# Kernel optimization log

Measured on AMD Instinct MI355X. Metric: run time of the kernel, lower is better.

## Reference

```python
import math
import jax, jax.numpy as jnp
import numpy as np

B = 65536
EMBED = 256
COND = 256
TIME = 128
HID = 256
E = 8
RHID = 128
IN_DIM = EMBED + TIME + COND  # 640


def setup_inputs() -> dict:
    key = jax.random.key(0)
    ks = jax.random.split(key, 20)
    s = 0.02
    inp = {
        "z_t": jax.random.normal(ks[0], (B, EMBED), jnp.float32),
        "t": jax.random.uniform(ks[1], (B, 1), jnp.float32),
        "cond": jax.random.normal(ks[2], (B, COND), jnp.float32),
        # time embedding proj (Linear(time,time) -> SiLU -> Linear(time,time))
        "tW1": jax.random.normal(ks[3], (TIME, TIME), jnp.float32) * s,
        "tb1": jnp.zeros((TIME,), jnp.float32),
        "tW2": jax.random.normal(ks[4], (TIME, TIME), jnp.float32) * s,
        "tb2": jnp.zeros((TIME,), jnp.float32),
        # stacked expert weights [E, in, out]
        "eW1": jax.random.normal(ks[5], (E, IN_DIM, HID), jnp.float32) * s,
        "eb1": jnp.zeros((E, HID), jnp.float32),
        "eW2": jax.random.normal(ks[6], (E, HID, HID), jnp.float32) * s,
        "eb2": jnp.zeros((E, HID), jnp.float32),
        "eW3": jax.random.normal(ks[7], (E, HID, EMBED), jnp.float32) * s,
        "eb3": jnp.zeros((E, EMBED), jnp.float32),
        # router
        "rW1": jax.random.normal(ks[8], (IN_DIM, RHID), jnp.float32) * s,
        "rb1": jnp.zeros((RHID,), jnp.float32),
        "rW2": jax.random.normal(ks[9], (RHID, E), jnp.float32) * s,
        "rb2": jnp.zeros((E,), jnp.float32),
    }
    return inp


def _time_embedding(t, tW1, tb1, tW2, tb2):
    half = TIME // 2  # 64
    scale = -math.log(10000.0) / (half - 1)
    freqs = jnp.exp(jnp.arange(half, dtype=t.dtype) * scale)[None, :]  # [1, half]
    angles = t * freqs  # [B, half]
    emb = jnp.concatenate([jnp.sin(angles), jnp.cos(angles)], axis=-1)  # [B, TIME]
    h = jax.nn.silu(emb @ tW1 + tb1)
    return h @ tW2 + tb2


def reference(z_t, t, cond, tW1, tb1, tW2, tb2, eW1, eb1, eW2, eb2, eW3, eb3, rW1, rb1, rW2, rb2):
    time_emb = _time_embedding(t, tW1, tb1, tW2, tb2)
    x = jnp.concatenate([z_t, time_emb, cond], axis=-1)  # [B, IN_DIM]
    # dense MoE: all experts via batched GEMMs (dropout=0 -> identity)
    h1 = jax.nn.silu(jnp.einsum('bi,eih->beh', x, eW1) + eb1)      # [B,E,HID]
    h2 = jax.nn.silu(jnp.einsum('beh,ehk->bek', h1, eW2) + eb2)    # [B,E,HID]
    expert_out = jnp.einsum('beh,ehd->bed', h2, eW3) + eb3         # [B,E,EMBED]
    # router softmax gate
    rh = jax.nn.silu(x @ rW1 + rb1)
    gate = jax.nn.softmax(rh @ rW2 + rb2, axis=-1)                 # [B,E]
    velocity = jnp.einsum('be,bed->bd', gate, expert_out)          # [B,EMBED]
    return velocity, gate
```

## Files before the change

kernel.cpp:

```cpp
#include <hip/hip_runtime.h>

typedef __attribute__((ext_vector_type(8))) short bf16x8;
typedef __attribute__((ext_vector_type(4))) float f32x4;

#define NB_ROWS 65536
#define D_EMBED 256
#define D_HID   256
#define N_EXP   8
#define D_RHID  128
#define D_IN    640
#define D_H1    2048

#define HSTR 264

static __device__ __forceinline__ ushort f2bf(float f) {
  union { float f; unsigned u; } v; v.f = f;
  unsigned r = v.u + 0x7fffu + ((v.u >> 16) & 1u);
  return (ushort)(r >> 16);
}
static __device__ __forceinline__ float bf2f(ushort h) {
  union { unsigned u; float f; } v; v.u = ((unsigned)h) << 16;
  return v.f;
}
static __device__ __forceinline__ float silu_f(float x) {
  return x / (1.0f + __expf(-x));
}

static __device__ __forceinline__ int kswz(int r, int c) {
  return r * 64 + ((((c) >> 3) ^ (r & 7)) << 3) + ((c) & 7);
}
static __device__ __forceinline__ int gswz(int r, int c) {
  return ((c) & ~63) | (((((c) >> 3) & 7) ^ ((r) & 7)) << 3) | ((c) & 7);
}

static __device__ __forceinline__ void gl16(const ushort* src, ushort* dst) {
  __builtin_amdgcn_global_load_lds(
      (const __attribute__((address_space(1))) void*)src,
      (__attribute__((address_space(3))) void*)dst, 16, 0, 0);
}

__global__ void prep_all(const float* __restrict__ tW1, const float* __restrict__ tW2,
                         const float* __restrict__ rW1, const float* __restrict__ eW1,
                         const float* __restrict__ eW2, const float* __restrict__ eW3,
                         ushort* __restrict__ tw1t, ushort* __restrict__ tw2t,
                         ushort* __restrict__ rw1t, ushort* __restrict__ w1t,
                         ushort* __restrict__ w2t, ushort* __restrict__ w3t) {
  int gidx = blockIdx.x * 256 + threadIdx.x;
  if (gidx >= 2473984) return;
  const float* src; ushort* dst; int R, C; int swz; int idx;
  if (gidx < 16384)        { src = tW1; dst = tw1t; R = 128; C = 128; swz = 0; idx = gidx; }
  else if (gidx < 32768)   { src = tW2; dst = tw2t; R = 128; C = 128; swz = 0; idx = gidx - 16384; }
  else if (gidx < 114688)  { src = rW1; dst = rw1t; R = 640; C = 128; swz = 1; idx = gidx - 32768; }
  else if (gidx < 1425408) { src = eW1; dst = w1t;  R = 640; C = 256; swz = 1; idx = gidx - 114688; }
  else if (gidx < 1949696) { src = eW2; dst = w2t;  R = 256; C = 256; swz = 1; idx = gidx - 1425408; }
  else                     { src = eW3; dst = w3t;  R = 256; C = 256; swz = 1; idx = gidx - 1949696; }
  int rc = R * C;
  int m = idx / rc;
  int rem = idx - m * rc;
  int r = rem / C;
  int c = rem - r * C;
  int p = swz ? ((r & ~63) + (((((r >> 3) & 7) ^ (c & 7)) << 3) | (r & 7))) : r;
  dst[m * rc + c * R + p] = f2bf(src[idx]);
}

static __device__ __forceinline__ void glB128_256(const ushort* __restrict__ src, int ld,
                                                  int kt, ushort* dst, int tid, int w) {
  #pragma unroll
  for (int c = 0; c < 4; ++c) {
    int f = c * 4096 + tid * 16;
    int r = f >> 7, ce = (f & 127) >> 1;
    gl16(src + (size_t)r * ld + kt + ce, dst + ((c * 4096 + w * 1024) >> 1));
  }
}

__global__ __launch_bounds__(512) void time_x_kernel(
    const float* __restrict__ zt, const float* __restrict__ tin,
    const float* __restrict__ cond,
    const ushort* __restrict__ tw1t, const ushort* __restrict__ tw2t,
    const float* __restrict__ tb1, const float* __restrict__ tb2,
    ushort* __restrict__ x) {
  __shared__ __align__(16) ushort sE[128 * 136];
  __shared__ float sFreq[64];
  __shared__ float sB1[128];
  __shared__ float sB2[128];

  const int tid = threadIdx.x;
  const int row0 = blockIdx.x * 128;

  for (int ch = tid; ch < 128 * 64; ch += 512) {
    int r = ch >> 6;
    int c4 = (ch & 63) << 2;
    size_t grow = (size_t)(row0 + r);
    float4 zv = *(const float4*)&zt[grow * 256 + c4];
    ushort4 o; o.x = f2bf(zv.x); o.y = f2bf(zv.y); o.z = f2bf(zv.z); o.w = f2bf(zv.w);
    *(ushort4*)&x[grow * 640 + gswz(r, c4)] = o;
    float4 cv = *(const float4*)&cond[grow * 256 + c4];
    ushort4 o2; o2.x = f2bf(cv.x); o2.y = f2bf(cv.y); o2.z = f2bf(cv.z); o2.w = f2bf(cv.w);
    *(ushort4*)&x[grow * 640 + gswz(r, 384 + c4)] = o2;
  }

  if (tid < 64) sFreq[tid] = __expf((float)tid * (-9.210340371976184f / 63.0f));
  if (tid < 128) { sB1[tid] = tb1[tid]; sB2[tid] = tb2[tid]; }
  __syncthreads();

  {
    int r = tid >> 2;
    int qd = tid & 3;
    float tv = tin[row0 + r];
    int half = qd >> 1;
    int cbase = (qd & 1) * 32;
    ushort* er = &sE[r * 136 + half * 64 + cbase];
    #pragma unroll
    for (int c = 0; c < 32; ++c) {
      float a = tv * sFreq[cbase + c];
      float v = half ? __cosf(a) : __sinf(a);
      er[c] = f2bf(v);
    }
  }
  __syncthreads();

  const int l = tid & 63;
  const int w = tid >> 6;
  const int wm = w >> 1;
  const int wn = w & 1;
  const int lr = l & 15;
  const int lk = (l >> 4) * 8;
  const int q4 = (l >> 4) * 4;

  f32x4 acc[2][4] = {};
  #pragma unroll
  for (int kk = 0; kk < 4; ++kk) {
    int kb = kk * 32 + lk;
    bf16x8 av[2], bv[4];
    #pragma unroll
    for (int mf = 0; mf < 2; ++mf)
      av[mf] = *(const bf16x8*)&sE[(wm * 32 + mf * 16 + lr) * 136 + kb];
    #pragma unroll
    for (int nf = 0; nf < 4; ++nf)
      bv[nf] = *(const bf16x8*)&tw1t[(size_t)(wn * 64 + nf * 16 + lr) * 128 + kb];
    #pragma unroll
    for (int mf = 0; mf < 2; ++mf)
      #pragma unroll
      for (int nf = 0; nf < 4; ++nf)
        acc[mf][nf] = __builtin_amdgcn_mfma_f32_16x16x32_bf16(av[mf], bv[nf], acc[mf][nf], 0, 0, 0);
  }
  __syncthreads();
  #pragma unroll
  for (int mf = 0; mf < 2; ++mf)
    #pragma unroll
    for (int nf = 0; nf < 4; ++nf) {
      int cc = wn * 64 + nf * 16 + lr;
      #pragma unroll
      for (int rg = 0; rg < 4; ++rg) {
        int rr = wm * 32 + mf * 16 + q4 + rg;
        sE[rr * 136 + cc] = f2bf(silu_f(acc[mf][nf][rg] + sB1[cc]));
      }
    }
  __syncthreads();

  f32x4 acc2[2][4] = {};
  #pragma unroll
  for (int kk = 0; kk < 4; ++kk) {
    int kb = kk * 32 + lk;
    bf16x8 av[2], bv[4];
    #pragma unroll
    for (int mf = 0; mf < 2; ++mf)
      av[mf] = *(const bf16x8*)&sE[(wm * 32 + mf * 16 + lr) * 136 + kb];
    #pragma unroll
    for (int nf = 0; nf < 4; ++nf)
      bv[nf] = *(const bf16x8*)&tw2t[(size_t)(wn * 64 + nf * 16 + lr) * 128 + kb];
    #pragma unroll
    for (int mf = 0; mf < 2; ++mf)
      #pragma unroll
      for (int nf = 0; nf < 4; ++nf)
        acc2[mf][nf] = __builtin_amdgcn_mfma_f32_16x16x32_bf16(av[mf], bv[nf], acc2[mf][nf], 0, 0, 0);
  }
  #pragma unroll
  for (int mf = 0; mf < 2; ++mf)
    #pragma unroll
    for (int nf = 0; nf < 4; ++nf) {
      int cc = wn * 64 + nf * 16 + lr;
      #pragma unroll
      for (int rg = 0; rg < 4; ++rg) {
        int rr = wm * 32 + mf * 16 + q4 + rg;
        x[(size_t)(row0 + rr) * 640 + gswz(rr, 256 + cc)] = f2bf(acc2[mf][nf][rg] + sB2[cc]);
      }
    }
}

__global__ __launch_bounds__(256) void router_kernel(
    const ushort* __restrict__ xb, const ushort* __restrict__ rw1t,
    const float* __restrict__ rb1, const float* __restrict__ rW2,
    const float* __restrict__ rb2, float* __restrict__ gatef,
    float* __restrict__ gateo) {
  __shared__ __align__(16) ushort smA[128 * 64];
  __shared__ __align__(16) ushort smB[128 * 64];
  __shared__ __align__(16) ushort rhbuf[128 * 136];
  __shared__ float sW2[128 * 8];

  const int tid = threadIdx.x;
  const int row0 = blockIdx.x * 128;
  for (int i = tid; i < 1024; i += 256) sW2[i] = rW2[i];

  const int l = tid & 63;
  const int w = tid >> 6;
  const int wm = w >> 1, wn = w & 1;
  const int lr = l & 15, lk = (l >> 4) * 8, q4 = (l >> 4) * 4;
  const ushort* xrow = xb + (size_t)row0 * 640;

  f32x4 acc[4][4] = {};
  for (int kt = 0; kt < 640; kt += 64) {
    glB128_256(xrow, 640, kt, smA, tid, w);
    glB128_256(rw1t, 640, kt, smB, tid, w);
    __syncthreads();
    #pragma unroll
    for (int kk = 0; kk < 2; ++kk) {
      int kb = kk * 32 + lk;
      bf16x8 av[4], bv[4];
      #pragma unroll
      for (int mf = 0; mf < 4; ++mf)
        av[mf] = *(const bf16x8*)&smA[kswz(wm * 64 + mf * 16 + lr, kb)];
      #pragma unroll
      for (int nf = 0; nf < 4; ++nf)
        bv[nf] = *(const bf16x8*)&smB[kswz(wn * 64 + nf * 16 + lr, kb)];
      #pragma unroll
      for (int mf = 0; mf < 4; ++mf)
        #pragma unroll
        for (int nf = 0; nf < 4; ++nf)
          acc[mf][nf] = __builtin_amdgcn_mfma_f32_16x16x32_bf16(av[mf], bv[nf], acc[mf][nf], 0, 0, 0);
    }
    __syncthreads();
  }
  #pragma unroll
  for (int nf = 0; nf < 4; ++nf) {
    int cc = wn * 64 + nf * 16 + lr;
    float b1v = rb1[cc];
    #pragma unroll
    for (int mf = 0; mf < 4; ++mf)
      #pragma unroll
      for (int rg = 0; rg < 4; ++rg) {
        int rr = wm * 64 + mf * 16 + q4 + rg;
        rhbuf[rr * 136 + cc] = f2bf(silu_f(acc[mf][nf][rg] + b1v));
      }
  }
  __syncthreads();

  if (tid < 128) {
    float a[8];
    #pragma unroll
    for (int e = 0; e < 8; ++e) a[e] = rb2[e];
    #pragma unroll
    for (int i8 = 0; i8 < 16; ++i8) {
      bf16x8 hv = *(const bf16x8*)&rhbuf[tid * 136 + i8 * 8];
      #pragma unroll
      for (int j = 0; j < 8; ++j) {
        float h = bf2f((ushort)hv[j]);
        const float* wrow = &sW2[(i8 * 8 + j) * 8];
        #pragma unroll
        for (int e = 0; e < 8; ++e) a[e] += h * wrow[e];
      }
    }
    float mx = a[0];
    #pragma unroll
    for (int e = 1; e < 8; ++e) mx = fmaxf(mx, a[e]);
    float s = 0.f, ex[8];
    #pragma unroll
    for (int e = 0; e < 8; ++e) { ex[e] = __expf(a[e] - mx); s += ex[e]; }
    float inv = 1.f / s;
    size_t b = (size_t)(row0 + tid);
    #pragma unroll
    for (int e = 0; e < 8; ++e) {
      float g = ex[e] * inv;
      gatef[b * 8 + e] = g;
      gateo[b * 8 + e] = g;
    }
  }
}

__global__ __launch_bounds__(512) void moe_h1_kernel(
    const ushort* __restrict__ xb, const ushort* __restrict__ w1t,
    const float* __restrict__ eb1, ushort* __restrict__ hg, int row_base) {
  __shared__ __align__(16) ushort smA[128 * 64];
  __shared__ __align__(16) ushort smB[256 * 64];

  const int tid = threadIdx.x;
  int nwg = gridDim.x;
  int flat = blockIdx.x;
  int sid = (flat & 7) * (nwg >> 3) + (flat >> 3);
  const int rb = sid >> 3;
  const int e  = sid & 7;
  const int lrow0 = rb * 128;

  const int l = tid & 63;
  const int w = tid >> 6;
  const int wm = w >> 2, wn = w & 3;
  const int lr = l & 15, lk = (l >> 4) * 8, q4 = (l >> 4) * 4;

  const ushort* xrow = xb + (size_t)(row_base + lrow0) * 640;
  const ushort* W1 = w1t + (size_t)e * (256 * 640);

  const ushort* aS[2]; ushort* aD[2];
  #pragma unroll
  for (int c = 0; c < 2; ++c) {
    int f = c * 8192 + tid * 16;
    int r = f >> 7, ce = (f & 127) >> 1;
    aS[c] = xrow + (size_t)r * 640 + ce;
    aD[c] = smA + ((c * 8192 + w * 1024) >> 1);
  }
  const ushort* bS[4]; ushort* bD[4];
  #pragma unroll
  for (int c = 0; c < 4; ++c) {
    int f = c * 8192 + tid * 16;
    int r = f >> 7, ce = (f & 127) >> 1;
    bS[c] = W1 + (size_t)r * 640 + ce;
    bD[c] = smB + ((c * 8192 + w * 1024) >> 1);
  }
  int oA[2][4], oB[2][4];
  #pragma unroll
  for (int kk = 0; kk < 2; ++kk) {
    #pragma unroll
    for (int mf = 0; mf < 4; ++mf) oA[kk][mf] = kswz(wm * 64 + mf * 16 + lr, kk * 32 + lk);
    #pragma unroll
    for (int nf = 0; nf < 4; ++nf) oB[kk][nf] = kswz(wn * 64 + nf * 16 + lr, kk * 32 + lk);
  }

  f32x4 acc[4][4] = {};
  for (int kt = 0; kt < 640; kt += 64) {
    #pragma unroll
    for (int c = 0; c < 2; ++c) { gl16(aS[c], aD[c]); aS[c] += 64; }
    #pragma unroll
    for (int c = 0; c < 4; ++c) { gl16(bS[c], bD[c]); bS[c] += 64; }
    __syncthreads();
    #pragma unroll
    for (int kk = 0; kk < 2; ++kk) {
      bf16x8 av[4], bv[4];
      #pragma unroll
      for (int mf = 0; mf < 4; ++mf) av[mf] = *(const bf16x8*)&smA[oA[kk][mf]];
      #pragma unroll
      for (int nf = 0; nf < 4; ++nf) bv[nf] = *(const bf16x8*)&smB[oB[kk][nf]];
      #pragma unroll
      for (int mf = 0; mf < 4; ++mf)
        #pragma unroll
        for (int nf = 0; nf < 4; ++nf)
          acc[mf][nf] = __builtin_amdgcn_mfma_f32_16x16x32_bf16(av[mf], bv[nf], acc[mf][nf], 0, 0, 0);
    }
    __syncthreads();
  }
  #pragma unroll
  for (int nf = 0; nf < 4; ++nf) {
    int cc = wn * 64 + nf * 16 + lr;
    float b1v = eb1[e * 256 + cc];
    #pragma unroll
    for (int mf = 0; mf < 4; ++mf)
      #pragma unroll
      for (int rg = 0; rg < 4; ++rg) {
        int rr = wm * 64 + mf * 16 + q4 + rg;
        hg[(size_t)(lrow0 + rr) * D_H1 + e * 256 + gswz(rr, cc)] =
            f2bf(silu_f(acc[mf][nf][rg] + b1v));
      }
  }
}

__global__ __launch_bounds__(512) void moe_h2_kernel(
    ushort* __restrict__ hg, const ushort* __restrict__ w2t,
    const float* __restrict__ eb2, const float* __restrict__ gatef, int row_base) {
  __shared__ __align__(16) ushort smA[128 * 64];
  __shared__ __align__(16) ushort smB[256 * 64];
  __shared__ float sGate[128];

  const int tid = threadIdx.x;
  int nwg = gridDim.x;
  int flat = blockIdx.x;
  int sid = (flat & 7) * (nwg >> 3) + (flat >> 3);
  const int rb = sid >> 3;
  const int e  = sid & 7;
  const int lrow0 = rb * 128;

  const int l = tid & 63;
  const int w = tid >> 6;
  const int wm = w >> 2, wn = w & 3;
  const int lr = l & 15, lk = (l >> 4) * 8, q4 = (l >> 4) * 4;

  if (tid < 128) sGate[tid] = gatef[(size_t)(row_base + lrow0 + tid) * 8 + e];

  ushort* hrow = hg + (size_t)lrow0 * D_H1 + e * 256;
  const ushort* W2 = w2t + (size_t)e * (256 * 256);

  const ushort* aS[2]; ushort* aD[2];
  #pragma unroll
  for (int c = 0; c < 2; ++c) {
    int f = c * 8192 + tid * 16;
    int r = f >> 7, ce = (f & 127) >> 1;
    aS[c] = hrow + (size_t)r * D_H1 + ce;
    aD[c] = smA + ((c * 8192 + w * 1024) >> 1);
  }
  const ushort* bS[4]; ushort* bD[4];
  #pragma unroll
  for (int c = 0; c < 4; ++c) {
    int f = c * 8192 + tid * 16;
    int r = f >> 7, ce = (f & 127) >> 1;
    bS[c] = W2 + (size_t)r * 256 + ce;
    bD[c] = smB + ((c * 8192 + w * 1024) >> 1);
  }
  int oA[2][4], oB[2][4];
  #pragma unroll
  for (int kk = 0; kk < 2; ++kk) {
    #pragma unroll
    for (int mf = 0; mf < 4; ++mf) oA[kk][mf] = kswz(wm * 64 + mf * 16 + lr, kk * 32 + lk);
    #pragma unroll
    for (int nf = 0; nf < 4; ++nf) oB[kk][nf] = kswz(wn * 64 + nf * 16 + lr, kk * 32 + lk);
  }

  f32x4 acc[4][4] = {};
  for (int kt = 0; kt < 256; kt += 64) {
    #pragma unroll
    for (int c = 0; c < 2; ++c) { gl16(aS[c], aD[c]); aS[c] += 64; }
    #pragma unroll
    for (int c = 0; c < 4; ++c) { gl16(bS[c], bD[c]); bS[c] += 64; }
    __syncthreads();
    #pragma unroll
    for (int kk = 0; kk < 2; ++kk) {
      bf16x8 av[4], bv[4];
      #pragma unroll
      for (int mf = 0; mf < 4; ++mf) av[mf] = *(const bf16x8*)&smA[oA[kk][mf]];
      #pragma unroll
      for (int nf = 0; nf < 4; ++nf) bv[nf] = *(const bf16x8*)&smB[oB[kk][nf]];
      #pragma unroll
      for (int mf = 0; mf < 4; ++mf)
        #pragma unroll
        for (int nf = 0; nf < 4; ++nf)
          acc[mf][nf] = __builtin_amdgcn_mfma_f32_16x16x32_bf16(av[mf], bv[nf], acc[mf][nf], 0, 0, 0);
    }
    __syncthreads();
  }
  #pragma unroll
  for (int nf = 0; nf < 4; ++nf) {
    int cc = wn * 64 + nf * 16 + lr;
    float b2v = eb2[e * 256 + cc];
    #pragma unroll
    for (int mf = 0; mf < 4; ++mf)
      #pragma unroll
      for (int rg = 0; rg < 4; ++rg) {
        int rr = wm * 64 + mf * 16 + q4 + rg;
        hrow[(size_t)rr * D_H1 + gswz(rr, cc)] =
            f2bf(silu_f(acc[mf][nf][rg] + b2v) * sGate[rr]);
      }
  }
}

__global__ __launch_bounds__(512) void moe_vel_kernel(
    const ushort* __restrict__ hg, const ushort* __restrict__ w3t,
    const float* __restrict__ eb3, const float* __restrict__ gatef,
    float* __restrict__ velout, int row_base) {
  __shared__ __align__(16) ushort smA[64 * 64];
  __shared__ __align__(16) ushort smB[256 * 64];
  __shared__ float sGate[64 * 8];

  const int tid = threadIdx.x;
  int nwg = gridDim.x;
  int flat = blockIdx.x;
  int sid = (flat & 7) * (nwg >> 3) + (flat >> 3);
  const int lrow0 = sid * 64;

  const int l = tid & 63;
  const int w = tid >> 6;
  const int wm = w >> 2, wn = w & 3;
  const int lr = l & 15, lk = (l >> 4) * 8, q4 = (l >> 4) * 4;

  if (tid < 512) sGate[tid] = gatef[(size_t)(row_base + lrow0) * 8 + tid];

  const ushort* hrow = hg + (size_t)lrow0 * D_H1;

  const ushort* aS; ushort* aD;
  {
    int f = tid * 16;
    int r = f >> 7, ce = (f & 127) >> 1;
    aS = hrow + (size_t)r * D_H1 + ce;
    aD = smA + ((tid * 16) >> 1);
  }
  int bR[4], bC[4]; ushort* bD[4];
  #pragma unroll
  for (int c = 0; c < 4; ++c) {
    int f = c * 8192 + tid * 16;
    bR[c] = f >> 7; bC[c] = (f & 127) >> 1;
    bD[c] = smB + ((c * 8192 + w * 1024) >> 1);
  }
  int oA[2][2], oB[2][4];
  #pragma unroll
  for (int kk = 0; kk < 2; ++kk) {
    #pragma unroll
    for (int mf = 0; mf < 2; ++mf) oA[kk][mf] = kswz(wm * 32 + mf * 16 + lr, kk * 32 + lk);
    #pragma unroll
    for (int nf = 0; nf < 4; ++nf) oB[kk][nf] = kswz(wn * 64 + nf * 16 + lr, kk * 32 + lk);
  }

  f32x4 vacc[2][4] = {};
  __syncthreads();

  for (int e = 0; e < 8; ++e) {
    const ushort* bS[4];
    const ushort* W3 = w3t + (size_t)e * (256 * 256);
    #pragma unroll
    for (int c = 0; c < 4; ++c) bS[c] = W3 + (size_t)bR[c] * 256 + bC[c];
    #pragma unroll
    for (int t4 = 0; t4 < 4; ++t4) {
      gl16(aS, aD); aS += 64;
      #pragma unroll
      for (int c = 0; c < 4; ++c) { gl16(bS[c], bD[c]); bS[c] += 64; }
      __syncthreads();
      #pragma unroll
      for (int kk = 0; kk < 2; ++kk) {
        bf16x8 av[2], bv[4];
        #pragma unroll
        for (int mf = 0; mf < 2; ++mf) av[mf] = *(const bf16x8*)&smA[oA[kk][mf]];
        #pragma unroll
        for (int nf = 0; nf < 4; ++nf) bv[nf] = *(const bf16x8*)&smB[oB[kk][nf]];
        #pragma unroll
        for (int mf = 0; mf < 2; ++mf)
          #pragma unroll
          for (int nf = 0; nf < 4; ++nf)
            vacc[mf][nf] = __builtin_amdgcn_mfma_f32_16x16x32_bf16(av[mf], bv[nf], vacc[mf][nf], 0, 0, 0);
      }
      __syncthreads();
    }
  }

  float* eL = (float*)smB;
  for (int i = tid; i < 2048; i += 512) eL[i] = eb3[i];
  __syncthreads();
  #pragma unroll
  for (int mf = 0; mf < 2; ++mf)
    #pragma unroll
    for (int rg = 0; rg < 4; ++rg) {
      int rr = wm * 32 + mf * 16 + q4 + rg;
      const float* gp = &sGate[rr * 8];
      #pragma unroll
      for (int nf = 0; nf < 4; ++nf) {
        int cc = wn * 64 + nf * 16 + lr;
        float bsum = 0.f;
        #pragma unroll
        for (int ee = 0; ee < 8; ++ee) bsum += gp[ee] * eL[ee * 256 + cc];
        velout[(size_t)(row_base + lrow0 + rr) * D_EMBED + cc] = vacc[mf][nf][rg] + bsum;
      }
    }
}

__global__ __launch_bounds__(512) void moe_fused_kernel(
    const ushort* __restrict__ xb, const ushort* __restrict__ w1t,
    const ushort* __restrict__ w2t, const ushort* __restrict__ w3t,
    const float* __restrict__ eb1, const float* __restrict__ eb2,
    const float* __restrict__ eb3, const float* __restrict__ gatef,
    float* __restrict__ velout) {
  __shared__ __align__(16) ushort smA[128 * 64];
  __shared__ __align__(16) ushort smB[256 * 64];
  __shared__ __align__(16) ushort hbuf[128 * HSTR];
  __shared__ float sGate[128 * 8];
  __shared__ float sEb3[8 * 256];

  const int tid = threadIdx.x;
  const int row0 = blockIdx.x * 128;
  const int l = tid & 63;
  const int w = tid >> 6;
  const int wm = w >> 2, wn = w & 3;
  const int lr = l & 15, lk = (l >> 4) * 8, q4 = (l >> 4) * 4;

  for (int i = tid; i < 1024; i += 512) sGate[i] = gatef[(size_t)row0 * 8 + i];
  for (int i = tid; i < 2048; i += 512) sEb3[i] = eb3[i];

  const ushort* xrow = xb + (size_t)row0 * 640;
  f32x4 vacc[4][4] = {};
  __syncthreads();

  for (int e = 0; e < 8; ++e) {
    const ushort* W1 = w1t + (size_t)e * (256 * 640);
    const ushort* W2 = w2t + (size_t)e * (256 * 256);
    const ushort* W3 = w3t + (size_t)e * (256 * 256);

    f32x4 acc[4][4] = {};
    for (int kt = 0; kt < 640; kt += 64) {
      #pragma unroll
      for (int c = 0; c < 2; ++c) {
        int f = c * 8192 + tid * 16;
        int r = f >> 7, ce = (f & 127) >> 1;
        gl16(xrow + (size_t)r * 640 + kt + ce, smA + ((c * 8192 + w * 1024) >> 1));
      }
      #pragma unroll
      for (int c = 0; c < 4; ++c) {
        int f = c * 8192 + tid * 16;
        int r = f >> 7, ce = (f & 127) >> 1;
        gl16(W1 + (size_t)r * 640 + kt + ce, smB + ((c * 8192 + w * 1024) >> 1));
      }
      __syncthreads();
      #pragma unroll
      for (int kk = 0; kk < 2; ++kk) {
        int kb = kk * 32 + lk;
        bf16x8 av[4], bv[4];
        #pragma unroll
        for (int mf = 0; mf < 4; ++mf)
          av[mf] = *(const bf16x8*)&smA[kswz(wm * 64 + mf * 16 + lr, kb)];
        #pragma unroll
        for (int nf = 0; nf < 4; ++nf)
          bv[nf] = *(const bf16x8*)&smB[kswz(wn * 64 + nf * 16 + lr, kb)];
        #pragma unroll
        for (int mf = 0; mf < 4; ++mf)
          #pragma unroll
          for (int nf = 0; nf < 4; ++nf)
            acc[mf][nf] = __builtin_amdgcn_mfma_f32_16x16x32_bf16(av[mf], bv[nf], acc[mf][nf], 0, 0, 0);
      }
      __syncthreads();
    }
    #pragma unroll
    for (int nf = 0; nf < 4; ++nf) {
      int cc = wn * 64 + nf * 16 + lr;
      float b1v = eb1[e * 256 + cc];
      #pragma unroll
      for (int mf = 0; mf < 4; ++mf)
        #pragma unroll
        for (int rg = 0; rg < 4; ++rg) {
          int rr = wm * 64 + mf * 16 + q4 + rg;
          hbuf[rr * HSTR + cc] = f2bf(silu_f(acc[mf][nf][rg] + b1v));
        }
    }
    __syncthreads();

    #pragma unroll
    for (int mf = 0; mf < 4; ++mf)
      #pragma unroll
      for (int nf = 0; nf < 4; ++nf)
        acc[mf][nf] = (f32x4){0.f, 0.f, 0.f, 0.f};
    for (int kt = 0; kt < 256; kt += 64) {
      #pragma unroll
      for (int c = 0; c < 4; ++c) {
        int f = c * 8192 + tid * 16;
        int r = f >> 7, ce = (f & 127) >> 1;
        gl16(W2 + (size_t)r * 256 + kt + ce, smB + ((c * 8192 + w * 1024) >> 1));
      }
      __syncthreads();
      #pragma unroll
      for (int kk = 0; kk < 2; ++kk) {
        int kbl = kk * 32 + lk;
        int kbh = kt + kbl;
        bf16x8 av[4], bv[4];
        #pragma unroll
        for (int mf = 0; mf < 4; ++mf)
          av[mf] = *(const bf16x8*)&hbuf[(wm * 64 + mf * 16 + lr) * HSTR + kbh];
        #pragma unroll
        for (int nf = 0; nf < 4; ++nf)
          bv[nf] = *(const bf16x8*)&smB[kswz(wn * 64 + nf * 16 + lr, kbl)];
        #pragma unroll
        for (int mf = 0; mf < 4; ++mf)
          #pragma unroll
          for (int nf = 0; nf < 4; ++nf)
            acc[mf][nf] = __builtin_amdgcn_mfma_f32_16x16x32_bf16(av[mf], bv[nf], acc[mf][nf], 0, 0, 0);
      }
      __syncthreads();
    }
    #pragma unroll
    for (int nf = 0; nf < 4; ++nf) {
      int cc = wn * 64 + nf * 16 + lr;
      float b2v = eb2[e * 256 + cc];
      #pragma unroll
      for (int mf = 0; mf < 4; ++mf)
        #pragma unroll
        for (int rg = 0; rg < 4; ++rg) {
          int rr = wm * 64 + mf * 16 + q4 + rg;
          float gv = sGate[rr * 8 + e];
          hbuf[rr * HSTR + cc] = f2bf(silu_f(acc[mf][nf][rg] + b2v) * gv);
        }
    }
    __syncthreads();

    for (int kt = 0; kt < 256; kt += 64) {
      #pragma unroll
      for (int c = 0; c < 4; ++c) {
        int f = c * 8192 + tid * 16;
        int r = f >> 7, ce = (f & 127) >> 1;
        gl16(W3 + (size_t)r * 256 + kt + ce, smB + ((c * 8192 + w * 1024) >> 1));
      }
      __syncthreads();
      #pragma unroll
      for (int kk = 0; kk < 2; ++kk) {
        int kbl = kk * 32 + lk;
        int kbh = kt + kbl;
        bf16x8 av[4], bv[4];
        #pragma unroll
        for (int mf = 0; mf < 4; ++mf)
          av[mf] = *(const bf16x8*)&hbuf[(wm * 64 + mf * 16 + lr) * HSTR + kbh];
        #pragma unroll
        for (int nf = 0; nf < 4; ++nf)
          bv[nf] = *(const bf16x8*)&smB[kswz(wn * 64 + nf * 16 + lr, kbl)];
        #pragma unroll
        for (int mf = 0; mf < 4; ++mf)
          #pragma unroll
          for (int nf = 0; nf < 4; ++nf)
            vacc[mf][nf] = __builtin_amdgcn_mfma_f32_16x16x32_bf16(av[mf], bv[nf], vacc[mf][nf], 0, 0, 0);
      }
      __syncthreads();
    }
  }

  #pragma unroll
  for (int mf = 0; mf < 4; ++mf)
    #pragma unroll
    for (int rg = 0; rg < 4; ++rg) {
      int rr = wm * 64 + mf * 16 + q4 + rg;
      const float* gp = &sGate[rr * 8];
      #pragma unroll
      for (int nf = 0; nf < 4; ++nf) {
        int cc = wn * 64 + nf * 16 + lr;
        float bsum = 0.f;
        #pragma unroll
        for (int ee = 0; ee < 8; ++ee) bsum += gp[ee] * sEb3[ee * 256 + cc];
        velout[(size_t)(row0 + rr) * D_EMBED + cc] = vacc[mf][nf][rg] + bsum;
      }
    }
}

extern "C" void kernel_launch(void* const* d_in, const int* in_sizes, int n_in,
                              void* d_out, int out_size, void* d_ws, size_t ws_size,
                              hipStream_t stream) {
  const float* zt   = (const float*)d_in[0];
  const float* tin  = (const float*)d_in[1];
  const float* cond = (const float*)d_in[2];
  const float* tW1  = (const float*)d_in[3];
  const float* tb1  = (const float*)d_in[4];
  const float* tW2  = (const float*)d_in[5];
  const float* tb2  = (const float*)d_in[6];
  const float* eW1  = (const float*)d_in[7];
  const float* eb1  = (const float*)d_in[8];
  const float* eW2  = (const float*)d_in[9];
  const float* eb2  = (const float*)d_in[10];
  const float* eW3  = (const float*)d_in[11];
  const float* eb3  = (const float*)d_in[12];
  const float* rW1  = (const float*)d_in[13];
  const float* rb1  = (const float*)d_in[14];
  const float* rW2  = (const float*)d_in[15];
  const float* rb2  = (const float*)d_in[16];

  char* wp = (char*)d_ws;
  ushort* xb    = (ushort*)wp; wp += (size_t)NB_ROWS * D_IN * 2;
  float*  gatef = (float*)wp;  wp += (size_t)NB_ROWS * 8 * 4;
  ushort* w1t   = (ushort*)wp; wp += (size_t)N_EXP * D_HID * D_IN * 2;
  ushort* w2t   = (ushort*)wp; wp += (size_t)N_EXP * D_HID * D_HID * 2;
  ushort* w3t   = (ushort*)wp; wp += (size_t)N_EXP * D_HID * D_EMBED * 2;
  ushort* rw1t  = (ushort*)wp; wp += (size_t)D_RHID * D_IN * 2;
  ushort* tw1t  = (ushort*)wp; wp += (size_t)128 * 128 * 2;
  ushort* tw2t  = (ushort*)wp; wp += (size_t)128 * 128 * 2;
  ushort* hg    = (ushort*)wp;
  size_t base = (size_t)(wp - (char*)d_ws);

  int CH = 0;
  for (int cand = NB_ROWS; cand >= 8192; cand >>= 1) {
    if (base + (size_t)cand * D_H1 * 2 <= ws_size) { CH = cand; break; }
  }

  float* velout  = (float*)d_out;
  float* gateout = velout + (size_t)NB_ROWS * D_EMBED;

  prep_all<<<(2473984 + 255) / 256, 256, 0, stream>>>(
      tW1, tW2, rW1, eW1, eW2, eW3, tw1t, tw2t, rw1t, w1t, w2t, w3t);

  time_x_kernel<<<512, 512, 0, stream>>>(zt, tin, cond, tw1t, tw2t, tb1, tb2, xb);
  router_kernel<<<512, 256, 0, stream>>>(xb, rw1t, rb1, rW2, rb2, gatef, gateout);

  if (CH > 0) {
    for (int r0 = 0; r0 < NB_ROWS; r0 += CH) {
      moe_h1_kernel<<<(CH / 128) * 8, 512, 0, stream>>>(xb, w1t, eb1, hg, r0);
      moe_h2_kernel<<<(CH / 128) * 8, 512, 0, stream>>>(hg, w2t, eb2, gatef, r0);
      moe_vel_kernel<<<CH / 64, 512, 0, stream>>>(hg, w3t, eb3, gatef, velout, r0);
    }
  } else {
    moe_fused_kernel<<<512, 512, 0, stream>>>(xb, w1t, w2t, w3t,
                                              eb1, eb2, eb3, gatef, velout);
  }
}
```

Before: 621.1 us.

## Fuse expert layer-2 and layer-3 GEMMs into one kernel via LDS staging

Replaces the separate h2 and velocity kernels with one kernel. Each 64-row block computes the layer-2 output for each expert, keeps the gated SiLU result in shared memory, and feeds it straight into the layer-3 GEMM. This drops the write and re-read of the gated h2 activations through global memory and one kernel launch. In exchange it uses 256-thread blocks with a larger shared-memory footprint, which can lower occupancy, and it serialises the two GEMMs inside each block.

```diff
diff --git a/kernel.cpp b/kernel.cpp
--- a/kernel.cpp
+++ b/kernel.cpp
@@ -361,99 +361,14 @@
   }
 }
 
-__global__ __launch_bounds__(512) void moe_h2_kernel(
-    ushort* __restrict__ hg, const ushort* __restrict__ w2t,
-    const float* __restrict__ eb2, const float* __restrict__ gatef, int row_base) {
-  __shared__ __align__(16) ushort smA[128 * 64];
-  __shared__ __align__(16) ushort smB[256 * 64];
-  __shared__ float sGate[128];
-
-  const int tid = threadIdx.x;
-  int nwg = gridDim.x;
-  int flat = blockIdx.x;
-  int sid = (flat & 7) * (nwg >> 3) + (flat >> 3);
-  const int rb = sid >> 3;
-  const int e  = sid & 7;
-  const int lrow0 = rb * 128;
-
-  const int l = tid & 63;
-  const int w = tid >> 6;
-  const int wm = w >> 2, wn = w & 3;
-  const int lr = l & 15, lk = (l >> 4) * 8, q4 = (l >> 4) * 4;
-
-  if (tid < 128) sGate[tid] = gatef[(size_t)(row_base + lrow0 + tid) * 8 + e];
-
-  ushort* hrow = hg + (size_t)lrow0 * D_H1 + e * 256;
-  const ushort* W2 = w2t + (size_t)e * (256 * 256);
-
-  const ushort* aS[2]; ushort* aD[2];
-  #pragma unroll
-  for (int c = 0; c < 2; ++c) {
-    int f = c * 8192 + tid * 16;
-    int r = f >> 7, ce = (f & 127) >> 1;
-    aS[c] = hrow + (size_t)r * D_H1 + ce;
-    aD[c] = smA + ((c * 8192 + w * 1024) >> 1);
-  }
-  const ushort* bS[4]; ushort* bD[4];
-  #pragma unroll
-  for (int c = 0; c < 4; ++c) {
-    int f = c * 8192 + tid * 16;
-    int r = f >> 7, ce = (f & 127) >> 1;
-    bS[c] = W2 + (size_t)r * 256 + ce;
-    bD[c] = smB + ((c * 8192 + w * 1024) >> 1);
-  }
-  int oA[2][4], oB[2][4];
-  #pragma unroll
-  for (int kk = 0; kk < 2; ++kk) {
-    #pragma unroll
-    for (int mf = 0; mf < 4; ++mf) oA[kk][mf] = kswz(wm * 64 + mf * 16 + lr, kk * 32 + lk);
-    #pragma unroll
-    for (int nf = 0; nf < 4; ++nf) oB[kk][nf] = kswz(wn * 64 + nf * 16 + lr, kk * 32 + lk);
-  }
-
-  f32x4 acc[4][4] = {};
-  for (int kt = 0; kt < 256; kt += 64) {
-    #pragma unroll
-    for (int c = 0; c < 2; ++c) { gl16(aS[c], aD[c]); aS[c] += 64; }
-    #pragma unroll
-    for (int c = 0; c < 4; ++c) { gl16(bS[c], bD[c]); bS[c] += 64; }
-    __syncthreads();
-    #pragma unroll
-    for (int kk = 0; kk < 2; ++kk) {
-      bf16x8 av[4], bv[4];
-      #pragma unroll
-      for (int mf = 0; mf < 4; ++mf) av[mf] = *(const bf16x8*)&smA[oA[kk][mf]];
-      #pragma unroll
-      for (int nf = 0; nf < 4; ++nf) bv[nf] = *(const bf16x8*)&smB[oB[kk][nf]];
-      #pragma unroll
-      for (int mf = 0; mf < 4; ++mf)
-        #pragma unroll
-        for (int nf = 0; nf < 4; ++nf)
-          acc[mf][nf] = __builtin_amdgcn_mfma_f32_16x16x32_bf16(av[mf], bv[nf], acc[mf][nf], 0, 0, 0);
-    }
-    __syncthreads();
-  }
-  #pragma unroll
-  for (int nf = 0; nf < 4; ++nf) {
-    int cc = wn * 64 + nf * 16 + lr;
-    float b2v = eb2[e * 256 + cc];
-    #pragma unroll
-    for (int mf = 0; mf < 4; ++mf)
-      #pragma unroll
-      for (int rg = 0; rg < 4; ++rg) {
-        int rr = wm * 64 + mf * 16 + q4 + rg;
-        hrow[(size_t)rr * D_H1 + gswz(rr, cc)] =
-            f2bf(silu_f(acc[mf][nf][rg] + b2v) * sGate[rr]);
-      }
-  }
-}
-
-__global__ __launch_bounds__(512) void moe_vel_kernel(
-    const ushort* __restrict__ hg, const ushort* __restrict__ w3t,
+__global__ __launch_bounds__(256) void moe_h2vel_kernel(
+    const ushort* __restrict__ hg, const ushort* __restrict__ w2t,
+    const ushort* __restrict__ w3t, const float* __restrict__ eb2,
     const float* __restrict__ eb3, const float* __restrict__ gatef,
     float* __restrict__ velout, int row_base) {
-  __shared__ __align__(16) ushort smA[64 * 64];
-  __shared__ __align__(16) ushort smB[256 * 64];
+  __shared__ __align__(16) ushort smH[64 * 64];
+  __shared__ __align__(16) ushort smW[256 * 64];
+  __shared__ __align__(16) ushort g2b[64 * 256];
   __shared__ float sGate[64 * 8];
 
   const int tid = threadIdx.x;
@@ -463,60 +378,104 @@
   const int lrow0 = sid * 64;
 
   const int l = tid & 63;
-  const int w = tid >> 6;
-  const int wm = w >> 2, wn = w & 3;
-  const int lr = l & 15, lk = (l >> 4) * 8, q4 = (l >> 4) * 4;
-
-  if (tid < 512) sGate[tid] = gatef[(size_t)(row_base + lrow0) * 8 + tid];
+  const int w4 = tid >> 6;
+  const int lr = l & 15;
+  const int lk = (l >> 4) * 8;
+  const int q4 = (l >> 4) * 4;
+
+  for (int i = tid; i < 512; i += 256) sGate[i] = gatef[(size_t)(row_base + lrow0) * 8 + i];
 
   const ushort* hrow = hg + (size_t)lrow0 * D_H1;
 
-  const ushort* aS; ushort* aD;
-  {
-    int f = tid * 16;
-    int r = f >> 7, ce = (f & 127) >> 1;
-    aS = hrow + (size_t)r * D_H1 + ce;
-    aD = smA + ((tid * 16) >> 1);
-  }
-  int bR[4], bC[4]; ushort* bD[4];
-  #pragma unroll
-  for (int c = 0; c < 4; ++c) {
-    int f = c * 8192 + tid * 16;
+  int aR[2], aC[2]; ushort* aD[2];
+  #pragma unroll
+  for (int c = 0; c < 2; ++c) {
+    int f = c * 4096 + tid * 16;
+    aR[c] = f >> 7; aC[c] = (f & 127) >> 1;
+    aD[c] = smH + ((c * 4096 + w4 * 1024) >> 1);
+  }
+  int bR[8], bC[8]; ushort* bD[8];
+  #pragma unroll
+  for (int c = 0; c < 8; ++c) {
+    int f = c * 4096 + tid * 16;
     bR[c] = f >> 7; bC[c] = (f & 127) >> 1;
-    bD[c] = smB + ((c * 8192 + w * 1024) >> 1);
-  }
-  int oA[2][2], oB[2][4];
+    bD[c] = smW + ((c * 4096 + w4 * 1024) >> 1);
+  }
+  int oA[2][4], oB[2][4];
   #pragma unroll
   for (int kk = 0; kk < 2; ++kk) {
     #pragma unroll
-    for (int mf = 0; mf < 2; ++mf) oA[kk][mf] = kswz(wm * 32 + mf * 16 + lr, kk * 32 + lk);
-    #pragma unroll
-    for (int nf = 0; nf < 4; ++nf) oB[kk][nf] = kswz(wn * 64 + nf * 16 + lr, kk * 32 + lk);
-  }
-
-  f32x4 vacc[2][4] = {};
+    for (int mf = 0; mf < 4; ++mf) oA[kk][mf] = kswz(mf * 16 + lr, kk * 32 + lk);
+    #pragma unroll
+    for (int nf = 0; nf < 4; ++nf) oB[kk][nf] = kswz(w4 * 64 + nf * 16 + lr, kk * 32 + lk);
+  }
+  int oG[2][4];
+  #pragma unroll
+  for (int kk = 0; kk < 2; ++kk)
+    #pragma unroll
+    for (int mf = 0; mf < 4; ++mf) {
+      int rr = mf * 16 + lr;
+      oG[kk][mf] = rr * 256 + gswz(rr, kk * 32 + lk);
+    }
+
+  f32x4 vacc[4][4] = {};
   __syncthreads();
 
   for (int e = 0; e < 8; ++e) {
-    const ushort* bS[4];
+    const ushort* Ae = hrow + e * 256;
+    const ushort* W2 = w2t + (size_t)e * (256 * 256);
     const ushort* W3 = w3t + (size_t)e * (256 * 256);
-    #pragma unroll
-    for (int c = 0; c < 4; ++c) bS[c] = W3 + (size_t)bR[c] * 256 + bC[c];
-    #pragma unroll
-    for (int t4 = 0; t4 < 4; ++t4) {
-      gl16(aS, aD); aS += 64;
-      #pragma unroll
-      for (int c = 0; c < 4; ++c) { gl16(bS[c], bD[c]); bS[c] += 64; }
+
+    f32x4 acc[4][4] = {};
+    for (int kt = 0; kt < 256; kt += 64) {
+      #pragma unroll
+      for (int c = 0; c < 2; ++c) gl16(Ae + (size_t)aR[c] * D_H1 + kt + aC[c], aD[c]);
+      #pragma unroll
+      for (int c = 0; c < 8; ++c) gl16(W2 + (size_t)bR[c] * 256 + kt + bC[c], bD[c]);
       __syncthreads();
       #pragma unroll
       for (int kk = 0; kk < 2; ++kk) {
-        bf16x8 av[2], bv[4];
-        #pragma unroll
-        for (int mf = 0; mf < 2; ++mf) av[mf] = *(const bf16x8*)&smA[oA[kk][mf]];
-        #pragma unroll
-        for (int nf = 0; nf < 4; ++nf) bv[nf] = *(const bf16x8*)&smB[oB[kk][nf]];
-        #pragma unroll
-        for (int mf = 0; mf < 2; ++mf)
+        bf16x8 av[4], bv[4];
+        #pragma unroll
+        for (int mf = 0; mf < 4; ++mf) av[mf] = *(const bf16x8*)&smH[oA[kk][mf]];
+        #pragma unroll
+        for (int nf = 0; nf < 4; ++nf) bv[nf] = *(const bf16x8*)&smW[oB[kk][nf]];
+        #pragma unroll
+        for (int mf = 0; mf < 4; ++mf)
+          #pragma unroll
+          for (int nf = 0; nf < 4; ++nf)
+            acc[mf][nf] = __builtin_amdgcn_mfma_f32_16x16x32_bf16(av[mf], bv[nf], acc[mf][nf], 0, 0, 0);
+      }
+      __syncthreads();
+    }
+    #pragma unroll
+    for (int nf = 0; nf < 4; ++nf) {
+      int cc = w4 * 64 + nf * 16 + lr;
+      float b2v = eb2[e * 256 + cc];
+      #pragma unroll
+      for (int mf = 0; mf < 4; ++mf)
+        #pragma unroll
+        for (int rg = 0; rg < 4; ++rg) {
+          int rr = mf * 16 + q4 + rg;
+          g2b[rr * 256 + gswz(rr, cc)] =
+              f2bf(silu_f(acc[mf][nf][rg] + b2v) * sGate[rr * 8 + e]);
+        }
+    }
+    __syncthreads();
+
+    for (int kt = 0; kt < 256; kt += 64) {
+      #pragma unroll
+      for (int c = 0; c < 8; ++c) gl16(W3 + (size_t)bR[c] * 256 + kt + bC[c], bD[c]);
+      __syncthreads();
+      #pragma unroll
+      for (int kk = 0; kk < 2; ++kk) {
+        bf16x8 av[4], bv[4];
+        #pragma unroll
+        for (int mf = 0; mf < 4; ++mf) av[mf] = *(const bf16x8*)&g2b[oG[kk][mf] + kt];
+        #pragma unroll
+        for (int nf = 0; nf < 4; ++nf) bv[nf] = *(const bf16x8*)&smW[oB[kk][nf]];
+        #pragma unroll
+        for (int mf = 0; mf < 4; ++mf)
           #pragma unroll
           for (int nf = 0; nf < 4; ++nf)
             vacc[mf][nf] = __builtin_amdgcn_mfma_f32_16x16x32_bf16(av[mf], bv[nf], vacc[mf][nf], 0, 0, 0);
@@ -525,18 +484,18 @@
     }
   }
 
-  float* eL = (float*)smB;
-  for (int i = tid; i < 2048; i += 512) eL[i] = eb3[i];
+  float* eL = (float*)smH;
+  for (int i = tid; i < 2048; i += 256) eL[i] = eb3[i];
   __syncthreads();
   #pragma unroll
-  for (int mf = 0; mf < 2; ++mf)
+  for (int mf = 0; mf < 4; ++mf)
     #pragma unroll
     for (int rg = 0; rg < 4; ++rg) {
-      int rr = wm * 32 + mf * 16 + q4 + rg;
+      int rr = mf * 16 + q4 + rg;
       const float* gp = &sGate[rr * 8];
       #pragma unroll
       for (int nf = 0; nf < 4; ++nf) {
-        int cc = wn * 64 + nf * 16 + lr;
+        int cc = w4 * 64 + nf * 16 + lr;
         float bsum = 0.f;
         #pragma unroll
         for (int ee = 0; ee < 8; ++ee) bsum += gp[ee] * eL[ee * 256 + cc];
@@ -766,8 +725,8 @@
   if (CH > 0) {
     for (int r0 = 0; r0 < NB_ROWS; r0 += CH) {
       moe_h1_kernel<<<(CH / 128) * 8, 512, 0, stream>>>(xb, w1t, eb1, hg, r0);
-      moe_h2_kernel<<<(CH / 128) * 8, 512, 0, stream>>>(hg, w2t, eb2, gatef, r0);
-      moe_vel_kernel<<<CH / 64, 512, 0, stream>>>(hg, w3t, eb3, gatef, velout, r0);
+      moe_h2vel_kernel<<<CH / 64, 256, 0, stream>>>(hg, w2t, w3t, eb2, eb3, gatef,
+                                                    velout, r0);
     }
   } else {
     moe_fused_kernel<<<512, 512, 0, stream>>>(xb, w1t, w2t, w3t,
```

After: 831.6 us. 33.9% more time.
